# Optimization experiments

Measured on AMD Instinct MI355X. Metric: run time of the kernel, lower is better.

## Reference

```python
import jax, jax.numpy as jnp
import numpy as np

B, T, E, H, M2 = 8, 2048, 256, 2, 134
HD = E // H


def setup_inputs() -> dict:
    key = jax.random.key(0)
    ks = jax.random.split(key, 10)
    s = 0.02
    return {
        "X": jax.random.normal(ks[0], (B, T, E), dtype=jnp.float32),
        "Y": jax.random.uniform(ks[1], (B, M2), dtype=jnp.float32),
        "wpe": s * jax.random.normal(ks[2], (T, E), dtype=jnp.float32),
        "ln1_g": jnp.ones((E,), jnp.float32), "ln1_b": jnp.zeros((E,), jnp.float32),
        "attn_w": s * jax.random.normal(ks[3], (3 * E, E), dtype=jnp.float32),
        "attn_b": jnp.zeros((3 * E,), jnp.float32),
        "attnproj_w": s * jax.random.normal(ks[4], (E, E), dtype=jnp.float32),
        "attnproj_b": jnp.zeros((E,), jnp.float32),
        "ln2_g": jnp.ones((E,), jnp.float32), "ln2_b": jnp.zeros((E,), jnp.float32),
        "fc_w": s * jax.random.normal(ks[5], (2 * E, E), dtype=jnp.float32),
        "fc_b": jnp.zeros((2 * E,), jnp.float32),
        "mlpproj_w": s * jax.random.normal(ks[6], (E, 2 * E), dtype=jnp.float32),
        "mlpproj_b": jnp.zeros((E,), jnp.float32),
        "lnf_g": jnp.ones((E,), jnp.float32), "lnf_b": jnp.zeros((E,), jnp.float32),
        "head_w": s * jax.random.normal(ks[7], (M2, E), dtype=jnp.float32),
        "head_b": jnp.zeros((M2,), jnp.float32),
    }


def _ln(x, g, b, eps=1e-5):
    mu = x.mean(-1, keepdims=True)
    var = ((x - mu) ** 2).mean(-1, keepdims=True)
    return (x - mu) * jax.lax.rsqrt(var + eps) * g + b


def reference(X, Y, wpe, ln1_g, ln1_b, attn_w, attn_b, attnproj_w, attnproj_b,
              ln2_g, ln2_b, fc_w, fc_b, mlpproj_w, mlpproj_b, lnf_g, lnf_b,
              head_w, head_b):
    # positional ids = arange(T) -> wpe itself; cls ids = [0]*T/2 + [1]*T/2
    cls_ids = np.concatenate([np.zeros(T // 2, np.int32), np.ones(T // 2, np.int32)])
    x = X + wpe + wpe[cls_ids]                      # [B,T,E] (dropout = identity, eval)

    # single Block (n_layer=1), preceded by ReLU as in cross_mod loop
    x = jax.nn.relu(x)
    h = _ln(x, ln1_g, ln1_b)
    qkv = h @ attn_w.T + attn_b                     # [B,T,3E]
    q, k, v = jnp.split(qkv, 3, axis=-1)
    q, k, v = jax.nn.relu(q), jax.nn.relu(k), jax.nn.relu(v)
    split_heads = lambda t: t.reshape(B, T, H, HD).transpose(0, 2, 1, 3)
    q, k, v = split_heads(q), split_heads(k), split_heads(v)
    att = jnp.einsum('bhqd,bhkd->bhqk', q, k) * (1.0 / np.sqrt(HD))
    tril = jnp.tril(jnp.ones((T, T), dtype=bool))
    # masked_fill(-inf) then ReLU  ==  zero outside causal mask, ReLU inside
    att = jnp.where(tril, jax.nn.relu(att), 0.0)    # [B,H,T,T]
    y = jnp.einsum('bhqk,bhkd->bhqd', att, v)
    y = y.transpose(0, 2, 1, 3).reshape(B, T, E)
    x = x + (y @ attnproj_w.T + attnproj_b)

    h = _ln(x, ln2_g, ln2_b)
    x = x + (jax.nn.relu(h @ fc_w.T + fc_b) @ mlpproj_w.T + mlpproj_b)

    x = jax.nn.relu(x)
    x = _ln(x, lnf_g, lnf_b)
    x = jax.nn.relu(x)
    emb = x.mean(axis=1)                            # [B,E]
    logits = jax.nn.relu(emb @ head_w.T + head_b)   # [B,M2]

    loss1 = jnp.sqrt(jnp.mean((logits - Y) ** 2))
    e1, e2 = emb[:, : E // 2], emb[:, E // 2:]
    loss3 = jnp.sqrt(jnp.mean((e1 - e2) ** 2))
    loss = 50.0 * loss1 + loss3
    return (e1, e2, loss, loss1, loss3, logits)
```

## Files before the change

### kernel.cpp

```cpp
#include <hip/hip_runtime.h>
#include <hip/hip_bf16.h>

#define Bc 8
#define Tc 2048
#define Ec 256
#define Hc 2
#define HDc 128
#define Mrows (Bc*Tc)
#define M2c 134

using bfx8  = __attribute__((ext_vector_type(8))) __bf16;
using f32x4 = __attribute__((ext_vector_type(4))) float;

__device__ __forceinline__ void gll16(const __bf16* g, __bf16* lds) {
    __builtin_amdgcn_global_load_lds(
        (const __attribute__((address_space(1))) unsigned int*)g,
        (__attribute__((address_space(3))) unsigned int*)lds, 16, 0, 0);
}

__global__ __launch_bounds__(256) void embed_prep_k(const float* X, const float* wpe,
                                                    const float* g, const float* bb,
                                                    const float* attn_w, const float* apw,
                                                    const float* fcw, const float* mpw,
                                                    __bf16* wb, float* embsum,
                                                    __bf16* xres, __bf16* hb) {
    int m = blockIdx.x;
    int e = threadIdx.x;
    if (m < 2048) {
        int i = m * 256 + e;
        if (i < 196608)       wb[i] = (__bf16)attn_w[i];
        else if (i < 262144)  wb[i] = (__bf16)apw[i - 196608];
        else if (i < 393216)  wb[i] = (__bf16)fcw[i - 262144];
        else                  wb[i] = (__bf16)mpw[i - 393216];
        if (m < 8) embsum[m * 256 + e] = 0.f;
    }
    int t = m & (Tc - 1);
    float v = X[(size_t)m * Ec + e] + wpe[(size_t)t * Ec + e] + wpe[(size_t)(t >= 1024) * Ec + e];
    v = fmaxf(v, 0.f);
    xres[(size_t)m * Ec + e] = (__bf16)v;
    float s1 = v, s2 = v * v;
    #pragma unroll
    for (int o = 32; o; o >>= 1) { s1 += __shfl_xor(s1, o, 64); s2 += __shfl_xor(s2, o, 64); }
    __shared__ float a1[4], a2[4];
    int w = threadIdx.x >> 6;
    if ((threadIdx.x & 63) == 0) { a1[w] = s1; a2[w] = s2; }
    __syncthreads();
    float m1 = (a1[0] + a1[1] + a1[2] + a1[3]) * (1.f / 256.f);
    float m2 = (a2[0] + a2[1] + a2[2] + a2[3]) * (1.f / 256.f);
    float r = rsqrtf(m2 - m1 * m1 + 1e-5f);
    hb[(size_t)m * Ec + e] = (__bf16)((v - m1) * r * g[e] + bb[e]);
}

__global__ __launch_bounds__(256) void gemm_qkv(const __bf16* __restrict__ A,
                                                const __bf16* __restrict__ Bw,
                                                const float* __restrict__ bias,
                                                __bf16* __restrict__ Qb,
                                                __bf16* __restrict__ Kb,
                                                __bf16* __restrict__ Vb) {
    const int K = 256;
    __shared__ __bf16 As[128 * 64];
    __shared__ __bf16 Bs[128 * 64];
    const int tid = threadIdx.x, w = tid >> 6, l = tid & 63;
    const int m0 = blockIdx.y * 128, n0 = blockIdx.x * 128;
    const int wr = w >> 1, wc = w & 1;
    const int quad = l >> 4, col15 = l & 15;

    f32x4 acc[4][4];
    f32x4 zz = {0.f, 0.f, 0.f, 0.f};
    #pragma unroll
    for (int i = 0; i < 4; i++)
        #pragma unroll
        for (int j = 0; j < 4; j++) acc[i][j] = zz;

    const int lrow = l >> 3;
    const int pbs  = l & 7;

    for (int kb = 0; kb < K; kb += 64) {
        #pragma unroll
        for (int it = 0; it < 4; it++) {
            int chunk = w * 4 + it;
            int row = chunk * 8 + lrow;
            int lb = pbs ^ (row & 7);
            gll16(A  + (size_t)(m0 + row) * K + kb + lb * 8, As + chunk * 512);
            gll16(Bw + (size_t)(n0 + row) * K + kb + lb * 8, Bs + chunk * 512);
        }
        __syncthreads();
        #pragma unroll
        for (int ks = 0; ks < 2; ks++) {
            bfx8 af[4], bfr[4];
            #pragma unroll
            for (int rt = 0; rt < 4; rt++) {
                int row = wr * 64 + rt * 16 + col15;
                int pb = (ks * 4 + quad) ^ (row & 7);
                af[rt] = *(const bfx8*)(As + row * 64 + pb * 8);
            }
            #pragma unroll
            for (int ct = 0; ct < 4; ct++) {
                int row = wc * 64 + ct * 16 + col15;
                int pb = (ks * 4 + quad) ^ (row & 7);
                bfr[ct] = *(const bfx8*)(Bs + row * 64 + pb * 8);
            }
            #pragma unroll
            for (int rt = 0; rt < 4; rt++)
                #pragma unroll
                for (int ct = 0; ct < 4; ct++)
                    acc[rt][ct] = __builtin_amdgcn_mfma_f32_16x16x32_bf16(af[rt], bfr[ct], acc[rt][ct], 0, 0, 0);
        }
        __syncthreads();
    }

    #pragma unroll
    for (int rt = 0; rt < 4; rt++)
        #pragma unroll
        for (int ct = 0; ct < 4; ct++) {
            int mgb = m0 + wr * 64 + rt * 16 + quad * 4;
            int ng  = n0 + wc * 64 + ct * 16 + col15;
            float bsv = bias[ng];
            #pragma unroll
            for (int r = 0; r < 4; r++) {
                float val = fmaxf(acc[rt][ct][r] + bsv, 0.f);
                int mg = mgb + r;
                int sel = ng >> 8;
                int hh = (ng >> 7) & 1;
                int d = ng & 127;
                int bb = mg >> 11, tt = mg & (Tc - 1);
                size_t idx = ((size_t)((bb * 2 + hh) * Tc + tt)) * HDc + d;
                __bf16 bv = (__bf16)val;
                if (sel == 0) Qb[idx] = bv;
                else if (sel == 1) Kb[idx] = bv;
                else Vb[idx] = bv;
            }
        }
}

__global__ __launch_bounds__(256) void transpose_v(const unsigned short* Vb, unsigned short* Vt) {
    __shared__ unsigned short tile[64][66];
    int kt = blockIdx.x, dt = blockIdx.y, bh = blockIdx.z;
    int tid = threadIdx.x;
    int k0 = kt * 64, d0 = dt * 64;
    int rr = tid >> 4, cc = (tid & 15) * 4;
    #pragma unroll
    for (int p = 0; p < 4; p++) {
        int k = p * 16 + rr;
        const unsigned short* src = Vb + ((size_t)(bh * Tc + k0 + k)) * HDc + d0 + cc;
        ushort4 vv = *(const ushort4*)src;
        tile[k][cc] = vv.x; tile[k][cc + 1] = vv.y; tile[k][cc + 2] = vv.z; tile[k][cc + 3] = vv.w;
    }
    __syncthreads();
    #pragma unroll
    for (int p = 0; p < 4; p++) {
        int d = p * 16 + rr;
        unsigned short* dst = Vt + ((size_t)(bh * HDc + d0 + d)) * Tc + k0 + cc;
        ushort4 ov;
        ov.x = tile[cc][d]; ov.y = tile[cc + 1][d]; ov.z = tile[cc + 2][d]; ov.w = tile[cc + 3][d];
        *(ushort4*)dst = ov;
    }
}

__global__ __launch_bounds__(512, 4) void attn6_k(const __bf16* __restrict__ Qb,
                                                  const __bf16* __restrict__ Kb,
                                                  const __bf16* __restrict__ Vt,
                                                  __bf16* __restrict__ Y1,
                                                  __bf16* __restrict__ Y2,
                                                  __bf16* __restrict__ Y3,
                                                  __bf16* __restrict__ Y4) {
    __shared__ __bf16 Ks[2][64 * 128];
    __shared__ __bf16 Vs[2][64 * 128];
    __shared__ __bf16 Ss[128 * 64];
    int bid = blockIdx.x;
    int lane8 = bid & 7;
    int s = bid >> 3;
    int bh = ((s & 1) << 3) | lane8;
    int f = s >> 1;
    int qt, ch;
    if (f < 16)      { qt = 12 + (f >> 2);          ch = f & 3; }
    else if (f < 28) { int r = f - 16; int d3 = r / 3; qt = 8 + d3; ch = r - 3 * d3; }
    else if (f < 36) { qt = 4 + ((f - 28) >> 1);    ch = (f - 28) & 1; }
    else             { qt = f - 36;                 ch = 0; }
    int Q0 = qt * 128;
    int kts = ch * 8;
    int kte = min(kts + 8, 2 * qt + 2);

    int tid = threadIdx.x, w = tid >> 6, l = tid & 63;
    int quad = l >> 4, col15 = l & 15;
    const int lrowK = l >> 4, pbsK = l & 15;
    const int lrowV = l >> 3, pbsV = l & 7;

    __bf16* Qs = &Ks[0][0];
    #pragma unroll
    for (int it = 0; it < 4; it++) {
        int chunk = w * 4 + it;
        int row = chunk * 4 + lrowK;
        int lb = pbsK ^ (row & 7);
        gll16(Qb + ((size_t)(bh * Tc + Q0 + row)) * HDc + lb * 8, Qs + chunk * 512);
    }
    __syncthreads();
    bfx8 qf[4];
    #pragma unroll
    for (int ks = 0; ks < 4; ks++) {
        int row = w * 16 + col15;
        int pb = (ks * 4 + quad) ^ (row & 7);
        qf[ks] = *(const bfx8*)(Qs + row * 128 + pb * 8);
    }
    __syncthreads();

    f32x4 zz = {0.f, 0.f, 0.f, 0.f};
    f32x4 yacc[8];
    #pragma unroll
    for (int i = 0; i < 8; i++) yacc[i] = zz;

    auto stageKV = [&](int buf, int kt) {
        #pragma unroll
        for (int it = 0; it < 2; it++) {
            int chunk = w * 2 + it;
            int rowK = chunk * 4 + lrowK;
            int lbK = pbsK ^ (rowK & 7);
            gll16(Kb + ((size_t)(bh * Tc + kt * 64 + rowK)) * HDc + lbK * 8, Ks[buf] + chunk * 512);
            int rowV = chunk * 8 + lrowV;
            int lbV = pbsV ^ (rowV & 7);
            gll16(Vt + ((size_t)(bh * HDc + rowV)) * Tc + kt * 64 + lbV * 8, Vs[buf] + chunk * 512);
        }
    };

    stageKV(0, kts);
    int cur = 0;
    for (int kt = kts; kt < kte; kt++) {
        __syncthreads();
        if (kt + 1 < kte) stageKV(cur ^ 1, kt + 1);

        f32x4 sacc[4];
        #pragma unroll
        for (int i = 0; i < 4; i++) sacc[i] = zz;
        #pragma unroll
        for (int ks = 0; ks < 4; ks++) {
            #pragma unroll
            for (int ct = 0; ct < 4; ct++) {
                int row = ct * 16 + col15;
                int pb = (ks * 4 + quad) ^ (row & 7);
                bfx8 kf = *(const bfx8*)(Ks[cur] + row * 128 + pb * 8);
                sacc[ct] = __builtin_amdgcn_mfma_f32_16x16x32_bf16(qf[ks], kf, sacc[ct], 0, 0, 0);
            }
        }

        #pragma unroll
        for (int ct = 0; ct < 4; ct++) {
            int kl = ct * 16 + col15;
            int kg = kt * 64 + kl;
            int blk = kl >> 3, off = kl & 7;
            #pragma unroll
            for (int r = 0; r < 4; r++) {
                int qlw = w * 16 + quad * 4 + r;
                float val = (kg <= Q0 + qlw) ? fmaxf(sacc[ct][r], 0.f) : 0.f;
                int pb = blk ^ (qlw & 7);
                Ss[qlw * 64 + pb * 8 + off] = (__bf16)val;
            }
        }

        #pragma unroll
        for (int ks = 0; ks < 2; ks++) {
            int rowS = w * 16 + col15;
            int pbS = (ks * 4 + quad) ^ (rowS & 7);
            bfx8 sf = *(const bfx8*)(Ss + rowS * 64 + pbS * 8);
            #pragma unroll
            for (int dt = 0; dt < 8; dt++) {
                int row = dt * 16 + col15;
                int pb = (ks * 4 + quad) ^ (row & 7);
                bfx8 vf = *(const bfx8*)(Vs[cur] + row * 64 + pb * 8);
                yacc[dt] = __builtin_amdgcn_mfma_f32_16x16x32_bf16(sf, vf, yacc[dt], 0, 0, 0);
            }
        }
        cur ^= 1;
    }

    __bf16* Yp = (ch == 0) ? Y1 : (ch == 1) ? Y2 : (ch == 2) ? Y3 : Y4;
    int b = bh >> 1, h = bh & 1;
    const float sc = 0.08838834764831845f;
    #pragma unroll
    for (int dt = 0; dt < 8; dt++) {
        int d = dt * 16 + col15;
        #pragma unroll
        for (int r = 0; r < 4; r++) {
            int q = Q0 + w * 16 + quad * 4 + r;
            Yp[((size_t)(b * Tc + q)) * Ec + h * HDc + d] = (__bf16)(yacc[dt][r] * sc);
        }
    }
}

__global__ __launch_bounds__(512, 1) void mega_k(const __bf16* __restrict__ Y1,
                                                 const __bf16* __restrict__ Y2,
                                                 const __bf16* __restrict__ Y3,
                                                 const __bf16* __restrict__ Y4,
                                                 const __bf16* __restrict__ wap,
                                                 const float* __restrict__ apb,
                                                 const __bf16* __restrict__ xres,
                                                 const float* __restrict__ ln2_g,
                                                 const float* __restrict__ ln2_b,
                                                 const __bf16* __restrict__ wfc,
                                                 const float* __restrict__ fcb,
                                                 const __bf16* __restrict__ wmp,
                                                 const float* __restrict__ mpb,
                                                 const float* __restrict__ lnf_g,
                                                 const float* __restrict__ lnf_b,
                                                 float* __restrict__ embsum) {
    __shared__ __bf16 h2s[4 * 4096];
    __shared__ __bf16 fc64[8 * 4096];
    __shared__ __bf16 Bs[256 * 64];
    __shared__ float ps1[64][8], ps2[64][8];
    __shared__ float mus[64], rss[64];
    const int tid = threadIdx.x, w = tid >> 6, l = tid & 63;
    const int m0 = blockIdx.x * 64;
    const int quad = l >> 4, col15 = l & 15;
    const int lrow = l >> 3, pbs = l & 7;
    const int n0 = w * 32;
    f32x4 zz = {0.f, 0.f, 0.f, 0.f};

    const int nsum = (((m0 & (Tc - 1)) >> 6) + 8) >> 3;
    __bf16* As = fc64;

    const int arow_s = tid >> 3;
    const int ablk   = tid & 7;

    auto loadY = [&](int kb) -> bfx8 {
        size_t off = (size_t)(m0 + arow_s) * 256 + kb + ablk * 8;
        bfx8 a1 = *(const bfx8*)(Y1 + off);
        float tmp[8];
        #pragma unroll
        for (int jj = 0; jj < 8; jj++) tmp[jj] = (float)a1[jj];
        if (nsum > 1) { bfx8 aj = *(const bfx8*)(Y2 + off);
            #pragma unroll
            for (int jj = 0; jj < 8; jj++) tmp[jj] += (float)aj[jj]; }
        if (nsum > 2) { bfx8 aj = *(const bfx8*)(Y3 + off);
            #pragma unroll
            for (int jj = 0; jj < 8; jj++) tmp[jj] += (float)aj[jj]; }
        if (nsum > 3) { bfx8 aj = *(const bfx8*)(Y4 + off);
            #pragma unroll
            for (int jj = 0; jj < 8; jj++) tmp[jj] += (float)aj[jj]; }
        #pragma unroll
        for (int jj = 0; jj < 8; jj++) a1[jj] = (__bf16)tmp[jj];
        return a1;
    };

    f32x4 acc[4][2];
    #pragma unroll
    for (int rt = 0; rt < 4; rt++)
        #pragma unroll
        for (int ct = 0; ct < 2; ct++) acc[rt][ct] = zz;

    bfx8 av = loadY(0);

    for (int kb = 0; kb < 256; kb += 64) {
        __syncthreads();
        { int pb = ablk ^ (arow_s & 7);
          *(bfx8*)(As + arow_s * 64 + pb * 8) = av; }
        #pragma unroll
        for (int it = 0; it < 4; it++) {
            int chunk = w * 4 + it;
            int row = chunk * 8 + lrow;
            int lb = pbs ^ (row & 7);
            gll16(wap + (size_t)row * 256 + kb + lb * 8, Bs + chunk * 512);
        }
        bfx8 avn;
        if (kb < 192) avn = loadY(kb + 64);
        __syncthreads();
        #pragma unroll
        for (int ks = 0; ks < 2; ks++) {
            bfx8 af[4];
            #pragma unroll
            for (int rt = 0; rt < 4; rt++) {
                int ar = rt * 16 + col15;
                int apbk = (ks * 4 + quad) ^ (ar & 7);
                af[rt] = *(const bfx8*)(As + ar * 64 + apbk * 8);
            }
            #pragma unroll
            for (int ct = 0; ct < 2; ct++) {
                int br = n0 + ct * 16 + col15;
                int bpb = (ks * 4 + quad) ^ (br & 7);
                bfx8 bf = *(const bfx8*)(Bs + br * 64 + bpb * 8);
                #pragma unroll
                for (int rt = 0; rt < 4; rt++)
                    acc[rt][ct] = __builtin_amdgcn_mfma_f32_16x16x32_bf16(af[rt], bf, acc[rt][ct], 0, 0, 0);
            }
        }
        if (kb < 192) av = avn;
    }

    float xv[4][2][4];
    #pragma unroll
    for (int ct = 0; ct < 2; ct++) {
        int ng = n0 + ct * 16 + col15;
        float bsv = apb[ng];
        #pragma unroll
        for (int rt = 0; rt < 4; rt++)
            #pragma unroll
            for (int r = 0; r < 4; r++) {
                int mg = m0 + rt * 16 + quad * 4 + r;
                xv[rt][ct][r] = acc[rt][ct][r] + bsv + (float)xres[(size_t)mg * 256 + ng];
            }
    }
    #pragma unroll
    for (int rt = 0; rt < 4; rt++)
        #pragma unroll
        for (int r = 0; r < 4; r++) {
            float a  = xv[rt][0][r] + xv[rt][1][r];
            float b2 = xv[rt][0][r] * xv[rt][0][r] + xv[rt][1][r] * xv[rt][1][r];
            #pragma unroll
            for (int o = 1; o < 16; o <<= 1) { a += __shfl_xor(a, o, 64); b2 += __shfl_xor(b2, o, 64); }
            if (col15 == 0) { int row = rt * 16 + quad * 4 + r; ps1[row][w] = a; ps2[row][w] = b2; }
        }
    __syncthreads();
    {
        int row = tid >> 3, widx = tid & 7;
        float a = ps1[row][widx], b2 = ps2[row][widx];
        #pragma unroll
        for (int o = 1; o < 8; o <<= 1) { a += __shfl_xor(a, o, 64); b2 += __shfl_xor(b2, o, 64); }
        if ((l & 7) == 0) {
            float mu = a * (1.f / 256.f);
            float var = b2 * (1.f / 256.f) - mu * mu;
            mus[row] = mu; rss[row] = rsqrtf(var + 1e-5f);
        }
    }
    __syncthreads();
    #pragma unroll
    for (int ct = 0; ct < 2; ct++) {
        int ng = n0 + ct * 16 + col15;
        float gv = ln2_g[ng], bv = ln2_b[ng];
        int panel = ng >> 6, c = ng & 63;
        #pragma unroll
        for (int rt = 0; rt < 4; rt++)
            #pragma unroll
            for (int r = 0; r < 4; r++) {
                int row = rt * 16 + quad * 4 + r;
                float h = (xv[rt][ct][r] - mus[row]) * rss[row] * gv + bv;
                h2s[panel * 4096 + row * 64 + ((c >> 3) ^ (row & 7)) * 8 + (c & 7)] = (__bf16)h;
            }
    }

    for (int half = 0; half < 2; half++) {
        f32x4 acc2[4][2];
        #pragma unroll
        for (int rt = 0; rt < 4; rt++)
            #pragma unroll
            for (int ct = 0; ct < 2; ct++) acc2[rt][ct] = zz;
        for (int kb = 0; kb < 256; kb += 64) {
            __syncthreads();
            #pragma unroll
            for (int it = 0; it < 4; it++) {
                int chunk = w * 4 + it;
                int row = chunk * 8 + lrow;
                int lb = pbs ^ (row & 7);
                gll16(wfc + (size_t)(half * 256 + row) * 256 + kb + lb * 8, Bs + chunk * 512);
            }
            __syncthreads();
            int panel = kb >> 6;
            #pragma unroll
            for (int ks = 0; ks < 2; ks++) {
                bfx8 af[4];
                #pragma unroll
                for (int rt = 0; rt < 4; rt++) {
                    int ar = rt * 16 + col15;
                    int apbk = (ks * 4 + quad) ^ (ar & 7);
                    af[rt] = *(const bfx8*)(h2s + panel * 4096 + ar * 64 + apbk * 8);
                }
                #pragma unroll
                for (int ct = 0; ct < 2; ct++) {
                    int br = n0 + ct * 16 + col15;
                    int bpb = (ks * 4 + quad) ^ (br & 7);
                    bfx8 bf = *(const bfx8*)(Bs + br * 64 + bpb * 8);
                    #pragma unroll
                    for (int rt = 0; rt < 4; rt++)
                        acc2[rt][ct] = __builtin_amdgcn_mfma_f32_16x16x32_bf16(af[rt], bf, acc2[rt][ct], 0, 0, 0);
                }
            }
        }
        #pragma unroll
        for (int ct = 0; ct < 2; ct++) {
            int col = half * 256 + n0 + ct * 16 + col15;
            float bsv = fcb[col];
            int panel = col >> 6, c = col & 63;
            #pragma unroll
            for (int rt = 0; rt < 4; rt++)
                #pragma unroll
                for (int r = 0; r < 4; r++) {
                    int row = rt * 16 + quad * 4 + r;
                    float val = fmaxf(acc2[rt][ct][r] + bsv, 0.f);
                    fc64[panel * 4096 + row * 64 + ((c >> 3) ^ (row & 7)) * 8 + (c & 7)] = (__bf16)val;
                }
        }
    }

    #pragma unroll
    for (int rt = 0; rt < 4; rt++)
        #pragma unroll
        for (int ct = 0; ct < 2; ct++) acc[rt][ct] = zz;
    for (int kb = 0; kb < 512; kb += 64) {
        __syncthreads();
        #pragma unroll
        for (int it = 0; it < 4; it++) {
            int chunk = w * 4 + it;
            int row = chunk * 8 + lrow;
            int lb = pbs ^ (row & 7);
            gll16(wmp + (size_t)row * 512 + kb + lb * 8, Bs + chunk * 512);
        }
        __syncthreads();
        int panel = kb >> 6;
        #pragma unroll
        for (int ks = 0; ks < 2; ks++) {
            bfx8 af[4];
            #pragma unroll
            for (int rt = 0; rt < 4; rt++) {
                int ar = rt * 16 + col15;
                int apbk = (ks * 4 + quad) ^ (ar & 7);
                af[rt] = *(const bfx8*)(fc64 + panel * 4096 + ar * 64 + apbk * 8);
            }
            #pragma unroll
            for (int ct = 0; ct < 2; ct++) {
                int br = n0 + ct * 16 + col15;
                int bpb = (ks * 4 + quad) ^ (br & 7);
                bfx8 bf = *(const bfx8*)(Bs + br * 64 + bpb * 8);
                #pragma unroll
                for (int rt = 0; rt < 4; rt++)
                    acc[rt][ct] = __builtin_amdgcn_mfma_f32_16x16x32_bf16(af[rt], bf, acc[rt][ct], 0, 0, 0);
            }
        }
    }

    #pragma unroll
    for (int ct = 0; ct < 2; ct++) {
        int ng = n0 + ct * 16 + col15;
        float bsv = mpb[ng];
        #pragma unroll
        for (int rt = 0; rt < 4; rt++)
            #pragma unroll
            for (int r = 0; r < 4; r++)
                xv[rt][ct][r] = fmaxf(acc[rt][ct][r] + bsv + xv[rt][ct][r], 0.f);
    }
    #pragma unroll
    for (int rt = 0; rt < 4; rt++)
        #pragma unroll
        for (int r = 0; r < 4; r++) {
            float a  = xv[rt][0][r] + xv[rt][1][r];
            float b2 = xv[rt][0][r] * xv[rt][0][r] + xv[rt][1][r] * xv[rt][1][r];
            #pragma unroll
            for (int o = 1; o < 16; o <<= 1) { a += __shfl_xor(a, o, 64); b2 += __shfl_xor(b2, o, 64); }
            if (col15 == 0) { int row = rt * 16 + quad * 4 + r; ps1[row][w] = a; ps2[row][w] = b2; }
        }
    __syncthreads();
    {
        int row = tid >> 3, widx = tid & 7;
        float a = ps1[row][widx], b2 = ps2[row][widx];
        #pragma unroll
        for (int o = 1; o < 8; o <<= 1) { a += __shfl_xor(a, o, 64); b2 += __shfl_xor(b2, o, 64); }
        if ((l & 7) == 0) {
            float mu = a * (1.f / 256.f);
            float var = b2 * (1.f / 256.f) - mu * mu;
            mus[row] = mu; rss[row] = rsqrtf(var + 1e-5f);
        }
    }
    __syncthreads();
    #pragma unroll
    for (int ct = 0; ct < 2; ct++) {
        int ng = n0 + ct * 16 + col15;
        float gv = lnf_g[ng], bv = lnf_b[ng];
        float csum = 0.f;
        #pragma unroll
        for (int rt = 0; rt < 4; rt++)
            #pragma unroll
            for (int r = 0; r < 4; r++) {
                int row = rt * 16 + quad * 4 + r;
                float h = (xv[rt][ct][r] - mus[row]) * rss[row] * gv + bv;
                csum += fmaxf(h, 0.f);
            }
        csum += __shfl_xor(csum, 16, 64);
        csum += __shfl_xor(csum, 32, 64);
        if (quad == 0) atomicAdd(&embsum[(m0 >> 11) * 256 + ng], csum);
    }
}

__global__ __launch_bounds__(256) void final_k(const float* embsum, const float* Yt,
                                               const float* head_w, const float* head_b,
                                               float* out) {
    __shared__ float semb[2048];
    __shared__ float slog[1072];
    int tid = threadIdx.x;
    for (int i = tid; i < 2048; i += 256) semb[i] = embsum[i] * (1.f / 2048.f);
    __syncthreads();
    float part1 = 0.f;
    for (int idx = tid; idx < 1072; idx += 256) {
        int b = idx / M2c, n = idx - b * M2c;
        float acc = head_b[n];
        const float* wn = head_w + (size_t)n * Ec;
        const float* e = semb + b * Ec;
        #pragma unroll 8
        for (int k = 0; k < Ec; k++) acc += e[k] * wn[k];
        acc = fmaxf(acc, 0.f);
        slog[idx] = acc;
        float d = acc - Yt[idx];
        part1 += d * d;
    }
    float part3 = 0.f;
    for (int idx = tid; idx < 1024; idx += 256) {
        int b = idx >> 7, i = idx & 127;
        float d = semb[b * Ec + i] - semb[b * Ec + 128 + i];
        part3 += d * d;
    }
    #pragma unroll
    for (int o = 32; o; o >>= 1) { part1 += __shfl_xor(part1, o, 64); part3 += __shfl_xor(part3, o, 64); }
    __shared__ float r1[4], r3[4];
    int w = tid >> 6;
    if ((tid & 63) == 0) { r1[w] = part1; r3[w] = part3; }
    __syncthreads();
    float l1 = sqrtf((r1[0] + r1[1] + r1[2] + r1[3]) / 1072.f);
    float l3 = sqrtf((r3[0] + r3[1] + r3[2] + r3[3]) / 1024.f);
    for (int idx = tid; idx < 1024; idx += 256) {
        int b = idx >> 7, i = idx & 127;
        out[idx]        = semb[b * Ec + i];
        out[1024 + idx] = semb[b * Ec + 128 + i];
    }
    if (tid == 0) {
        out[2048] = 50.f * l1 + l3;
        out[2049] = l1;
        out[2050] = l3;
    }
    for (int idx = tid; idx < 1072; idx += 256) out[2051 + idx] = slog[idx];
}

extern "C" void kernel_launch(void* const* d_in, const int* in_sizes, int n_in,
                              void* d_out, int out_size, void* d_ws, size_t ws_size,
                              hipStream_t stream) {
    const float* X        = (const float*)d_in[0];
    const float* Yt       = (const float*)d_in[1];
    const float* wpe      = (const float*)d_in[2];
    const float* ln1_g    = (const float*)d_in[3];
    const float* ln1_b    = (const float*)d_in[4];
    const float* attn_w   = (const float*)d_in[5];
    const float* attn_b   = (const float*)d_in[6];
    const float* apw      = (const float*)d_in[7];
    const float* apb      = (const float*)d_in[8];
    const float* ln2_g    = (const float*)d_in[9];
    const float* ln2_b    = (const float*)d_in[10];
    const float* fcw      = (const float*)d_in[11];
    const float* fcb      = (const float*)d_in[12];
    const float* mpw      = (const float*)d_in[13];
    const float* mpb      = (const float*)d_in[14];
    const float* lnf_g    = (const float*)d_in[15];
    const float* lnf_b    = (const float*)d_in[16];
    const float* head_w   = (const float*)d_in[17];
    const float* head_b   = (const float*)d_in[18];

    char* ws = (char*)d_ws;
    const size_t MB = 1048576;
    __bf16* xres   = (__bf16*)(ws + 0 * MB);
    __bf16* hb     = (__bf16*)(ws + 8 * MB);
    __bf16* Qb     = (__bf16*)(ws + 16 * MB);
    __bf16* Kb     = (__bf16*)(ws + 24 * MB);
    __bf16* Vb     = (__bf16*)(ws + 32 * MB);
    __bf16* Vt     = (__bf16*)(ws + 40 * MB);
    __bf16* Y1     = (__bf16*)(ws + 48 * MB);
    __bf16* Y2     = (__bf16*)(ws + 56 * MB);
    __bf16* wb     = (__bf16*)(ws + 64 * MB);
    float*  embsum = (float*)(ws + 65 * MB);

    __bf16* Y3 = hb;
    __bf16* Y4 = Vb;

    __bf16* wqkv = wb;
    __bf16* wap  = wb + 196608;
    __bf16* wfc  = wb + 262144;
    __bf16* wmp  = wb + 393216;

    embed_prep_k<<<Mrows, 256, 0, stream>>>(X, wpe, ln1_g, ln1_b,
                                            attn_w, apw, fcw, mpw, wb, embsum, xres, hb);
    gemm_qkv<<<dim3(6, 128), 256, 0, stream>>>(hb, wqkv, attn_b, Qb, Kb, Vb);
    transpose_v<<<dim3(32, 2, 16), 256, 0, stream>>>((const unsigned short*)Vb, (unsigned short*)Vt);
    attn6_k<<<640, 512, 0, stream>>>(Qb, Kb, Vt, Y1, Y2, Y3, Y4);
    mega_k<<<256, 512, 0, stream>>>(Y1, Y2, Y3, Y4, wap, apb, xres, ln2_g, ln2_b,
                                    wfc, fcb, wmp, mpb, lnf_g, lnf_b, embsum);
    final_k<<<1, 256, 0, stream>>>(embsum, Yt, head_w, head_b, (float*)d_out);
}
```

Measured before the change: 234.5 us.

## Split attention warps into 2x2 query/key tiles for fragment reuse

The attention kernel's eight warps move from 16 query rows each over all keys to a 2x2 split: pairs of warps share 32 query rows and each half owns 32 keys for QK^T and 64 head dims for S·V. Each K and V fragment loaded from LDS now feeds two MFMAs, cutting LDS read traffic per MFMA. Because warps now write S entries that other warps read, an explicit LDS wait and barrier is added between the score write and the S·V phase. That is one more block-wide sync per key tile, and each warp holds twice the Q fragments in registers.

```diff
diff --git a/kernel.cpp b/kernel.cpp
--- a/kernel.cpp
+++ b/kernel.cpp
@@ -183,6 +183,7 @@
 
     int tid = threadIdx.x, w = tid >> 6, l = tid & 63;
     int quad = l >> 4, col15 = l & 15;
+    const int qs = w >> 1, kh = w & 1;
     const int lrowK = l >> 4, pbsK = l & 15;
     const int lrowV = l >> 3, pbsV = l & 7;
 
@@ -195,19 +196,23 @@
         gll16(Qb + ((size_t)(bh * Tc + Q0 + row)) * HDc + lb * 8, Qs + chunk * 512);
     }
     __syncthreads();
-    bfx8 qf[4];
-    #pragma unroll
-    for (int ks = 0; ks < 4; ks++) {
-        int row = w * 16 + col15;
-        int pb = (ks * 4 + quad) ^ (row & 7);
-        qf[ks] = *(const bfx8*)(Qs + row * 128 + pb * 8);
-    }
+    bfx8 qf[2][4];
+    #pragma unroll
+    for (int rt = 0; rt < 2; rt++)
+        #pragma unroll
+        for (int ks = 0; ks < 4; ks++) {
+            int row = qs * 32 + rt * 16 + col15;
+            int pb = (ks * 4 + quad) ^ (row & 7);
+            qf[rt][ks] = *(const bfx8*)(Qs + row * 128 + pb * 8);
+        }
     __syncthreads();
 
     f32x4 zz = {0.f, 0.f, 0.f, 0.f};
-    f32x4 yacc[8];
-    #pragma unroll
-    for (int i = 0; i < 8; i++) yacc[i] = zz;
+    f32x4 yacc[2][4];
+    #pragma unroll
+    for (int rt = 0; rt < 2; rt++)
+        #pragma unroll
+        for (int dt = 0; dt < 4; dt++) yacc[rt][dt] = zz;
 
     auto stageKV = [&](int buf, int kt) {
         #pragma unroll
@@ -228,45 +233,61 @@
         __syncthreads();
         if (kt + 1 < kte) stageKV(cur ^ 1, kt + 1);
 
-        f32x4 sacc[4];
-        #pragma unroll
-        for (int i = 0; i < 4; i++) sacc[i] = zz;
+        f32x4 sacc[2][2];
+        #pragma unroll
+        for (int rt = 0; rt < 2; rt++)
+            #pragma unroll
+            for (int ct = 0; ct < 2; ct++) sacc[rt][ct] = zz;
         #pragma unroll
         for (int ks = 0; ks < 4; ks++) {
             #pragma unroll
-            for (int ct = 0; ct < 4; ct++) {
-                int row = ct * 16 + col15;
+            for (int ct = 0; ct < 2; ct++) {
+                int row = kh * 32 + ct * 16 + col15;
                 int pb = (ks * 4 + quad) ^ (row & 7);
                 bfx8 kf = *(const bfx8*)(Ks[cur] + row * 128 + pb * 8);
-                sacc[ct] = __builtin_amdgcn_mfma_f32_16x16x32_bf16(qf[ks], kf, sacc[ct], 0, 0, 0);
-            }
-        }
-
-        #pragma unroll
-        for (int ct = 0; ct < 4; ct++) {
-            int kl = ct * 16 + col15;
+                #pragma unroll
+                for (int rt = 0; rt < 2; rt++)
+                    sacc[rt][ct] = __builtin_amdgcn_mfma_f32_16x16x32_bf16(qf[rt][ks], kf, sacc[rt][ct], 0, 0, 0);
+            }
+        }
+
+        #pragma unroll
+        for (int ct = 0; ct < 2; ct++) {
+            int kl = kh * 32 + ct * 16 + col15;
             int kg = kt * 64 + kl;
             int blk = kl >> 3, off = kl & 7;
             #pragma unroll
-            for (int r = 0; r < 4; r++) {
-                int qlw = w * 16 + quad * 4 + r;
-                float val = (kg <= Q0 + qlw) ? fmaxf(sacc[ct][r], 0.f) : 0.f;
-                int pb = blk ^ (qlw & 7);
-                Ss[qlw * 64 + pb * 8 + off] = (__bf16)val;
-            }
-        }
+            for (int rt = 0; rt < 2; rt++)
+                #pragma unroll
+                for (int r = 0; r < 4; r++) {
+                    int qlw = qs * 32 + rt * 16 + quad * 4 + r;
+                    float val = (kg <= Q0 + qlw) ? fmaxf(sacc[rt][ct][r], 0.f) : 0.f;
+                    int pb = blk ^ (qlw & 7);
+                    Ss[qlw * 64 + pb * 8 + off] = (__bf16)val;
+                }
+        }
+
+        asm volatile("s_waitcnt lgkmcnt(0)" ::: "memory");
+        __builtin_amdgcn_s_barrier();
+        __builtin_amdgcn_sched_barrier(0);
 
         #pragma unroll
         for (int ks = 0; ks < 2; ks++) {
-            int rowS = w * 16 + col15;
-            int pbS = (ks * 4 + quad) ^ (rowS & 7);
-            bfx8 sf = *(const bfx8*)(Ss + rowS * 64 + pbS * 8);
-            #pragma unroll
-            for (int dt = 0; dt < 8; dt++) {
-                int row = dt * 16 + col15;
-                int pb = (ks * 4 + quad) ^ (row & 7);
-                bfx8 vf = *(const bfx8*)(Vs[cur] + row * 64 + pb * 8);
-                yacc[dt] = __builtin_amdgcn_mfma_f32_16x16x32_bf16(sf, vf, yacc[dt], 0, 0, 0);
+            bfx8 sf[2];
+            #pragma unroll
+            for (int rt = 0; rt < 2; rt++) {
+                int rowS = qs * 32 + rt * 16 + col15;
+                int pbS = (ks * 4 + quad) ^ (rowS & 7);
+                sf[rt] = *(const bfx8*)(Ss + rowS * 64 + pbS * 8);
+            }
+            #pragma unroll
+            for (int dt = 0; dt < 4; dt++) {
+                int rowV = kh * 64 + dt * 16 + col15;
+                int pb = (ks * 4 + quad) ^ (rowV & 7);
+                bfx8 vf = *(const bfx8*)(Vs[cur] + rowV * 64 + pb * 8);
+                #pragma unroll
+                for (int rt = 0; rt < 2; rt++)
+                    yacc[rt][dt] = __builtin_amdgcn_mfma_f32_16x16x32_bf16(sf[rt], vf, yacc[rt][dt], 0, 0, 0);
             }
         }
         cur ^= 1;
@@ -276,14 +297,16 @@
     int b = bh >> 1, h = bh & 1;
     const float sc = 0.08838834764831845f;
     #pragma unroll
-    for (int dt = 0; dt < 8; dt++) {
-        int d = dt * 16 + col15;
-        #pragma unroll
-        for (int r = 0; r < 4; r++) {
-            int q = Q0 + w * 16 + quad * 4 + r;
-            Yp[((size_t)(b * Tc + q)) * Ec + h * HDc + d] = (__bf16)(yacc[dt][r] * sc);
-        }
-    }
+    for (int rt = 0; rt < 2; rt++)
+        #pragma unroll
+        for (int dt = 0; dt < 4; dt++) {
+            int d = kh * 64 + dt * 16 + col15;
+            #pragma unroll
+            for (int r = 0; r < 4; r++) {
+                int q = Q0 + qs * 32 + rt * 16 + quad * 4 + r;
+                Yp[((size_t)(b * Tc + q)) * Ec + h * HDc + d] = (__bf16)(yacc[rt][dt][r] * sc);
+            }
+        }
 }
 
 __global__ __launch_bounds__(512, 1) void mega_k(const __bf16* __restrict__ Y1,
```

New measurement: 234.4 us. About the same (-0.0%).
